# Kernel tuning notes

Hardware: AMD Instinct MI355X
Metric: run time of the kernel (lower is better)

Reference implementation:

```python
import jax, jax.numpy as jnp
import numpy as np

N = 100000
E = 1600000
IN_DIM = 128
HID = 128
OUT = 64
BN_EPS = 1e-5


def setup_inputs() -> dict:
    key = jax.random.key(0)
    ks = jax.random.split(key, 12)
    x = jax.random.normal(ks[0], (N, IN_DIM), dtype=jnp.float32)
    src = jax.random.randint(ks[1], (E,), 0, N, dtype=jnp.int64)
    dst = jax.random.randint(ks[2], (E,), 0, N, dtype=jnp.int64)
    edge_index = jnp.stack([src, dst], axis=0)
    def glorot(k, fan_in, fan_out):
        s = jnp.sqrt(6.0 / (fan_in + fan_out)).astype(jnp.float32)
        return jax.random.uniform(k, (fan_in, fan_out), jnp.float32, -s, s)
    return {
        "x": x,
        "edge_index": edge_index,
        "W1": glorot(ks[3], IN_DIM, HID), "b1": jnp.zeros((HID,), jnp.float32),
        "g1": jnp.ones((HID,), jnp.float32), "be1": jnp.zeros((HID,), jnp.float32),
        "W2": glorot(ks[4], HID, HID), "b2": jnp.zeros((HID,), jnp.float32),
        "g2": jnp.ones((HID,), jnp.float32), "be2": jnp.zeros((HID,), jnp.float32),
        "W3": glorot(ks[5], HID, OUT), "b3": jnp.zeros((OUT,), jnp.float32),
    }


def _gcn_norm(edge_index, n):
    # PyG GCNConv: add self-loops, symmetric normalization D^-1/2 (A+I) D^-1/2
    loop = jnp.arange(n, dtype=edge_index.dtype)
    src = jnp.concatenate([edge_index[0], loop])
    dst = jnp.concatenate([edge_index[1], loop])
    deg = jax.ops.segment_sum(jnp.ones_like(src, dtype=jnp.float32), dst, num_segments=n)
    dinv = jnp.where(deg > 0, jax.lax.rsqrt(deg), 0.0)
    norm = dinv[src] * dinv[dst]  # [E+N]
    return src, dst, norm


def _gcn(x, src, dst, norm, W, b, n):
    xw = x @ W                                  # [N, out]
    msg = xw[src] * norm[:, None]               # gather over edges
    return jax.ops.segment_sum(msg, dst, num_segments=n) + b


def _bn(x, g, be):
    # training-mode BatchNorm1d over node dim, biased variance
    mu = jnp.mean(x, axis=0)
    var = jnp.mean(jnp.square(x - mu), axis=0)
    return (x - mu) * jax.lax.rsqrt(var + BN_EPS) * g + be


def reference(x, edge_index, W1, b1, g1, be1, W2, b2, g2, be2, W3, b3):
    n = x.shape[0]
    src, dst, norm = _gcn_norm(edge_index, n)
    h = _gcn(x, src, dst, norm, W1, b1, n)
    h = jax.nn.relu(_bn(h, g1, be1))  # dropout = identity (eval)
    h = _gcn(h, src, dst, norm, W2, b2, n)
    h = jax.nn.relu(_bn(h, g2, be2))
    return _gcn(h, src, dst, norm, W3, b3, n)
```

## Files before the change

### kernel.cpp

```cpp
#include <hip/hip_runtime.h>
#include <cstdint>
#include <cstddef>

#define BN_EPS 1e-5f
#define BKT 256
#define BSH 9
#define CHUNK 8192

typedef __attribute__((ext_vector_type(8))) short bf16x8;
typedef __attribute__((ext_vector_type(4))) float f32x4;

__device__ __forceinline__ unsigned int f32_to_bf16_rne(float f) {
    unsigned int u = __float_as_uint(f);
    u += 0x7FFFu + ((u >> 16) & 1u);
    return u >> 16;
}
__device__ __forceinline__ unsigned int pack_bf16x2(float a, float b) {
    return f32_to_bf16_rne(a) | (f32_to_bf16_rne(b) << 16);
}
__device__ __forceinline__ float bf16_lo(unsigned int p) { return __uint_as_float(p << 16); }
__device__ __forceinline__ float bf16_hi(unsigned int p) { return __uint_as_float(p & 0xFFFF0000u); }

__global__ void hist_kernel(const int* __restrict__ dst, int* __restrict__ H, int e, int G) {
    __shared__ int h[BKT];
    int t = threadIdx.x, g = blockIdx.x;
    h[t] = 0;
    __syncthreads();
    int base = g * CHUNK;
#pragma unroll
    for (int i = 0; i < CHUNK / 256; i++) {
        int idx = base + i * 256 + t;
        if (idx < e) atomicAdd(&h[dst[idx] >> BSH], 1);
    }
    __syncthreads();
    H[t * G + g] = h[t];
}

__global__ void bin_scatter_kernel(const int* __restrict__ src, const int* __restrict__ dst,
                                   const int* __restrict__ Hscan, uint2* __restrict__ binned,
                                   int e, int G) {
    __shared__ int cur[BKT];
    int t = threadIdx.x, g = blockIdx.x;
    cur[t] = Hscan[t * G + g];
    __syncthreads();
    int base = g * CHUNK;
#pragma unroll
    for (int i = 0; i < CHUNK / 256; i++) {
        int idx = base + i * 256 + t;
        if (idx < e) {
            int s = src[idx], d = dst[idx];
            int pos = atomicAdd(&cur[d >> BSH], 1);
            uint2 v; v.x = (unsigned)s; v.y = (unsigned)d;
            binned[pos] = v;
        }
    }
}

__global__ __launch_bounds__(256) void bucket_build_kernel(const uint2* __restrict__ binned,
                                                           const int* __restrict__ Hscan,
                                                           int* __restrict__ cnt,
                                                           int* __restrict__ rowptr,
                                                           float* __restrict__ dinv,
                                                           int* __restrict__ esrc,
                                                           int e, int G, int n) {
    __shared__ int lcnt[512], lexc[512], ssum[256];
    const int t = threadIdx.x;
    const int b = blockIdx.x;
    const int start = Hscan[b * G];
    const int end = (b == BKT - 1) ? e : Hscan[(b + 1) * G];

    lcnt[t] = 0; lcnt[t + 256] = 0;
    __syncthreads();
    for (int i = start + t; i < end; i += 256)
        atomicAdd(&lcnt[binned[i].y & 511], 1);
    __syncthreads();

    int a0 = lcnt[2 * t], a1 = lcnt[2 * t + 1];
    ssum[t] = a0 + a1;
    __syncthreads();
    for (int off = 1; off < 256; off <<= 1) {
        int v = (t >= off) ? ssum[t - off] : 0;
        __syncthreads();
        ssum[t] += v;
        __syncthreads();
    }
    int excl = (t == 0) ? 0 : ssum[t - 1];
    lexc[2 * t] = excl;
    lexc[2 * t + 1] = excl + a0;
    __syncthreads();

    int nodebase = b << BSH;
#pragma unroll
    for (int j2 = 0; j2 < 2; j2++) {
        int j = 2 * t + j2;
        int node = nodebase + j;
        if (node < n) {
            int c = lcnt[j];
            cnt[node] = c;
            rowptr[node] = start + lexc[j];
            dinv[node] = rsqrtf((float)(c + 1));
        }
    }
    __syncthreads();

    for (int i = start + t; i < end; i += 256) {
        uint2 ed = binned[i];
        int pos = start + atomicAdd(&lexc[ed.y & 511], 1);
        esrc[pos] = (int)ed.x;
    }
}


__global__ void blocksum_kernel(const int* __restrict__ in, int* __restrict__ bsum, int n) {
    int t = threadIdx.x;
    int base = blockIdx.x * 1024 + t * 4;
    int s = 0;
    if (base + 3 < n) {
        int4 v = *(const int4*)&in[base];
        s = v.x + v.y + v.z + v.w;
    } else {
        for (int j = 0; j < 4; j++) if (base + j < n) s += in[base + j];
    }
    __shared__ int ls[256];
    ls[t] = s;
    __syncthreads();
    for (int off = 128; off > 0; off >>= 1) {
        if (t < off) ls[t] += ls[t + off];
        __syncthreads();
    }
    if (t == 0) bsum[blockIdx.x] = ls[0];
}

__global__ void scan_bsum_kernel(int* __restrict__ bsum, int nb) {
    int t = threadIdx.x;
    __shared__ int ls[256];
    int v = (t < nb) ? bsum[t] : 0;
    ls[t] = v;
    __syncthreads();
    for (int off = 1; off < 256; off <<= 1) {
        int p = (t >= off) ? ls[t - off] : 0;
        __syncthreads();
        ls[t] += p;
        __syncthreads();
    }
    if (t < nb) bsum[t] = ls[t] - v;
}

__global__ void scan_write1_kernel(const int* __restrict__ in, const int* __restrict__ bsum,
                                   int* __restrict__ out, int n) {
    int t = threadIdx.x;
    int base = blockIdx.x * 1024 + t * 4;
    int v[4];
    int s = 0;
    if (base + 3 < n) {
        int4 q = *(const int4*)&in[base];
        v[0] = q.x; v[1] = q.y; v[2] = q.z; v[3] = q.w;
        s = q.x + q.y + q.z + q.w;
    } else {
        for (int j = 0; j < 4; j++) { v[j] = (base + j < n) ? in[base + j] : 0; s += v[j]; }
    }
    __shared__ int ls[256];
    ls[t] = s;
    __syncthreads();
    for (int off = 1; off < 256; off <<= 1) {
        int p = (t >= off) ? ls[t - off] : 0;
        __syncthreads();
        ls[t] += p;
        __syncthreads();
    }
    int run = bsum[blockIdx.x] + ls[t] - s;
    if (base + 3 < n) {
        int4 r; r.x = run; r.y = run + v[0]; r.z = run + v[0] + v[1]; r.w = run + v[0] + v[1] + v[2];
        *(int4*)&out[base] = r;
    } else {
        for (int j = 0; j < 4; j++) {
            if (base + j < n) out[base + j] = run;
            run += v[j];
        }
    }
}


__device__ __forceinline__ void wprep_one(const float* __restrict__ W,
                                          uint4* __restrict__ whi, uint4* __restrict__ wlo,
                                          int slot, int OUTC) {
    int l  = slot & 63;
    int kc = (slot >> 6) & 3;
    int ct = slot >> 8;
    int c  = ct * 16 + (l & 15);
    int k0 = kc * 32 + (l >> 4) * 8;
    unsigned hi[4], lo[4];
#pragma unroll
    for (int jj = 0; jj < 4; jj++) {
        float v0 = W[(size_t)(k0 + 2 * jj) * OUTC + c];
        float v1 = W[(size_t)(k0 + 2 * jj + 1) * OUTC + c];
        unsigned h0 = f32_to_bf16_rne(v0), h1 = f32_to_bf16_rne(v1);
        float l0 = v0 - __uint_as_float(h0 << 16);
        float l1 = v1 - __uint_as_float(h1 << 16);
        hi[jj] = h0 | (h1 << 16);
        lo[jj] = pack_bf16x2(l0, l1);
    }
    uint4 uh; uh.x = hi[0]; uh.y = hi[1]; uh.z = hi[2]; uh.w = hi[3];
    uint4 ul; ul.x = lo[0]; ul.y = lo[1]; ul.z = lo[2]; ul.w = lo[3];
    whi[slot] = uh;
    wlo[slot] = ul;
}

__global__ void wprep_all_kernel(const float* __restrict__ W1, uint4* w1hi, uint4* w1lo,
                                 const float* __restrict__ W2, uint4* w2hi, uint4* w2lo,
                                 const float* __restrict__ W3, uint4* w3hi, uint4* w3lo) {
    int id = blockIdx.x * 256 + threadIdx.x;
    if (id < 2048)       wprep_one(W1, w1hi, w1lo, id, 128);
    else if (id < 4096)  wprep_one(W2, w2hi, w2lo, id - 2048, 128);
    else if (id < 5120)  wprep_one(W3, w3hi, w3lo, id - 4096, 64);
}


template <int OUTC>
__global__ __launch_bounds__(256) void gemm_kernel(const float* __restrict__ X,
                                                   const uint4* __restrict__ whi,
                                                   const uint4* __restrict__ wlo,
                                                   const float* __restrict__ scale,
                                                   const float* __restrict__ shift,
                                                   const float* __restrict__ dinv,
                                                   unsigned int* __restrict__ Y, int n) {
    constexpr int NCT = OUTC / 16;
    constexpr int CTW = NCT / 4;
    __shared__ __align__(16) unsigned short lAhi[64 * 128];
    __shared__ __align__(16) unsigned short lAlo[64 * 128];
    __shared__ float ldv[64];
    const int t = threadIdx.x;
    const int base = blockIdx.x * 64;
    const int lane = t & 63;
    const int w = t >> 6;
    const bool bn = (scale != nullptr);

    if (t < 64) { int r = base + t; ldv[t] = (r < n) ? dinv[r] : 0.0f; }

    bf16x8 bhi[CTW][4], blo[CTW][4];
#pragma unroll
    for (int c = 0; c < CTW; c++) {
        int ct = w * CTW + c;
#pragma unroll
        for (int kc = 0; kc < 4; kc++) {
            int slot = (ct * 4 + kc) * 64 + lane;
            bhi[c][kc] = *reinterpret_cast<const bf16x8*>(whi + slot);
            blo[c][kc] = *reinterpret_cast<const bf16x8*>(wlo + slot);
        }
    }

    const int col4 = (t & 31) * 4;
    float4 sc4, sh4;
    if (bn) {
        sc4 = *(const float4*)&scale[col4];
        sh4 = *(const float4*)&shift[col4];
    }
#pragma unroll
    for (int i = 0; i < 8; i++) {
        int row = i * 8 + (t >> 5);
        int r = base + row;
        float4 xv = make_float4(0.f, 0.f, 0.f, 0.f);
        if (r < n) xv = *(const float4*)&X[(size_t)r * 128 + col4];
        if (bn) {
            xv.x = fmaxf(fmaf(xv.x, sc4.x, sh4.x), 0.0f);
            xv.y = fmaxf(fmaf(xv.y, sc4.y, sh4.y), 0.0f);
            xv.z = fmaxf(fmaf(xv.z, sc4.z, sh4.z), 0.0f);
            xv.w = fmaxf(fmaf(xv.w, sc4.w, sh4.w), 0.0f);
        }
        unsigned h0 = f32_to_bf16_rne(xv.x), h1 = f32_to_bf16_rne(xv.y);
        unsigned h2 = f32_to_bf16_rne(xv.z), h3 = f32_to_bf16_rne(xv.w);
        float l0 = xv.x - __uint_as_float(h0 << 16);
        float l1 = xv.y - __uint_as_float(h1 << 16);
        float l2 = xv.z - __uint_as_float(h2 << 16);
        float l3 = xv.w - __uint_as_float(h3 << 16);
        uint2 ph; ph.x = h0 | (h1 << 16); ph.y = h2 | (h3 << 16);
        uint2 pl; pl.x = pack_bf16x2(l0, l1); pl.y = pack_bf16x2(l2, l3);
        int off = row * 256 + ((col4 * 2) ^ ((row & 7) << 4));
        *(uint2*)((char*)lAhi + off) = ph;
        *(uint2*)((char*)lAlo + off) = pl;
    }
    __syncthreads();

    const int arow = lane & 15;
    const int kb16 = (lane >> 4) * 16;
#pragma unroll
    for (int rt = 0; rt < 4; rt++) {
        f32x4 acc[CTW];
#pragma unroll
        for (int c = 0; c < CTW; c++) acc[c] = (f32x4){0.f, 0.f, 0.f, 0.f};
        int row = rt * 16 + arow;
        int rb = row * 256;
        int sw = (row & 7) << 4;
#pragma unroll
        for (int kc = 0; kc < 4; kc++) {
            int off = rb + ((kc * 64 + kb16) ^ sw);
            bf16x8 ah = *(const bf16x8*)((const char*)lAhi + off);
            bf16x8 al = *(const bf16x8*)((const char*)lAlo + off);
#pragma unroll
            for (int c = 0; c < CTW; c++) {
                acc[c] = __builtin_amdgcn_mfma_f32_16x16x32_bf16(bhi[c][kc], ah, acc[c], 0, 0, 0);
                acc[c] = __builtin_amdgcn_mfma_f32_16x16x32_bf16(blo[c][kc], ah, acc[c], 0, 0, 0);
                acc[c] = __builtin_amdgcn_mfma_f32_16x16x32_bf16(bhi[c][kc], al, acc[c], 0, 0, 0);
            }
        }
        int r = base + row;
        if (r < n) {
            float dv = ldv[row];
#pragma unroll
            for (int c = 0; c < CTW; c++) {
                int ct = w * CTW + c;
                uint2 o;
                o.x = pack_bf16x2(acc[c][0] * dv, acc[c][1] * dv);
                o.y = pack_bf16x2(acc[c][2] * dv, acc[c][3] * dv);
                *(uint2*)&Y[(size_t)r * (OUTC / 2) + ct * 8 + (lane >> 4) * 2] = o;
            }
        }
    }
}


__global__ __launch_bounds__(256) void agg128_kernel(const unsigned int* __restrict__ xw,
                                                     const int* __restrict__ rowptr,
                                                     const int* __restrict__ cnt,
                                                     const int* __restrict__ esrc,
                                                     const float* __restrict__ dinv,
                                                     const float* __restrict__ bias,
                                                     float* __restrict__ out,
                                                     float* __restrict__ bnpart, int n) {
    __shared__ float lp[8][128];
    __shared__ float lq[8][128];

    const uint2* xw2 = (const uint2*)xw;
    int wid = (blockIdx.x * 256 + threadIdx.x) >> 6;
    int lane = threadIdx.x & 63;
    int half = lane >> 5;
    int hl = lane & 31;
    int node = wid * 2 + half;
    bool ok = node < n;
    int nc = ok ? node : 0;

    float di = dinv[nc];
    int beg = rowptr[nc];
    int cv  = ok ? cnt[nc] : 0;
    int last = beg + cv - 1;
    int nb = (cv + 7) >> 3;

    uint2 ap = xw2[(size_t)nc * 32 + hl];
    float ax = bf16_lo(ap.x), ay = bf16_hi(ap.x);
    float az = bf16_lo(ap.y), aw = bf16_hi(ap.y);

    int s[8], sn[8];
    if (nb > 0) {
#pragma unroll
        for (int j = 0; j < 8; j++) {
            int idx = beg + j;
            s[j] = esrc[idx <= last ? idx : last];
        }
    }
    for (int b = 0; b < nb; b++) {
        int ebase = beg + b * 8;
        if (b + 1 < nb) {
#pragma unroll
            for (int j = 0; j < 8; j++) {
                int idx = ebase + 8 + j;
                sn[j] = esrc[idx <= last ? idx : last];
            }
        }
        uint2 v[8];
#pragma unroll
        for (int j = 0; j < 8; j++) v[j] = xw2[(size_t)s[j] * 32 + hl];
        int rem = last - ebase;
#pragma unroll
        for (int j = 0; j < 8; j++) {
            float m = (j <= rem) ? 1.0f : 0.0f;
            ax = fmaf(m, bf16_lo(v[j].x), ax);
            ay = fmaf(m, bf16_hi(v[j].x), ay);
            az = fmaf(m, bf16_lo(v[j].y), az);
            aw = fmaf(m, bf16_hi(v[j].y), aw);
        }
        if (b + 1 < nb) {
#pragma unroll
            for (int j = 0; j < 8; j++) s[j] = sn[j];
        }
    }

    float4 o = make_float4(0.f, 0.f, 0.f, 0.f);
    if (ok) {
        float4 bv = ((const float4*)bias)[hl];
        o.x = fmaf(di, ax, bv.x);
        o.y = fmaf(di, ay, bv.y);
        o.z = fmaf(di, az, bv.z);
        o.w = fmaf(di, aw, bv.w);
        ((float4*)(out + (size_t)node * 128))[hl] = o;
    }

    int row8 = (threadIdx.x >> 6) * 2 + half;
    int c0 = hl * 4;
    lp[row8][c0 + 0] = o.x;  lq[row8][c0 + 0] = o.x * o.x;
    lp[row8][c0 + 1] = o.y;  lq[row8][c0 + 1] = o.y * o.y;
    lp[row8][c0 + 2] = o.z;  lq[row8][c0 + 2] = o.z * o.z;
    lp[row8][c0 + 3] = o.w;  lq[row8][c0 + 3] = o.w * o.w;
    __syncthreads();
    int c = threadIdx.x & 127;
    int which = threadIdx.x >> 7;
    float srd = 0.0f;
#pragma unroll
    for (int r = 0; r < 8; r++) srd += which ? lq[r][c] : lp[r][c];
    bnpart[(size_t)blockIdx.x * 256 + threadIdx.x] = srd;
}


__global__ __launch_bounds__(256) void agg64_kernel(const unsigned int* __restrict__ xw,
                                                    const int* __restrict__ rowptr,
                                                    const int* __restrict__ cnt,
                                                    const int* __restrict__ esrc,
                                                    const float* __restrict__ dinv,
                                                    const float* __restrict__ bias,
                                                    float* __restrict__ out, int n) {
    int wid = (blockIdx.x * 256 + threadIdx.x) >> 6;
    int lane = threadIdx.x & 63;
    int half = lane >> 5;
    int hl = lane & 31;
    int node = wid * 2 + half;
    bool ok = node < n;
    int nc = ok ? node : 0;

    float di = dinv[nc];
    int beg = rowptr[nc];
    int cv  = ok ? cnt[nc] : 0;
    int last = beg + cv - 1;
    int nb = (cv + 7) >> 3;

    unsigned int ap = xw[(size_t)nc * 32 + hl];
    float ax = bf16_lo(ap), ay = bf16_hi(ap);

    int s[8], sn[8];
    if (nb > 0) {
#pragma unroll
        for (int j = 0; j < 8; j++) {
            int idx = beg + j;
            s[j] = esrc[idx <= last ? idx : last];
        }
    }
    for (int b = 0; b < nb; b++) {
        int ebase = beg + b * 8;
        if (b + 1 < nb) {
#pragma unroll
            for (int j = 0; j < 8; j++) {
                int idx = ebase + 8 + j;
                sn[j] = esrc[idx <= last ? idx : last];
            }
        }
        unsigned int v[8];
#pragma unroll
        for (int j = 0; j < 8; j++) v[j] = xw[(size_t)s[j] * 32 + hl];
        int rem = last - ebase;
#pragma unroll
        for (int j = 0; j < 8; j++) {
            float m = (j <= rem) ? 1.0f : 0.0f;
            ax = fmaf(m, bf16_lo(v[j]), ax);
            ay = fmaf(m, bf16_hi(v[j]), ay);
        }
        if (b + 1 < nb) {
#pragma unroll
            for (int j = 0; j < 8; j++) s[j] = sn[j];
        }
    }
    if (ok) {
        float2 bv = ((const float2*)bias)[hl];
        float2 o;
        o.x = fmaf(di, ax, bv.x);
        o.y = fmaf(di, ay, bv.y);
        ((float2*)(out + (size_t)node * 64))[hl] = o;
    }
}


__global__ void bnred_partial_kernel(const float* __restrict__ part, float* __restrict__ sums,
                                     int nblk) {
    int t = threadIdx.x;
    float s = 0.0f;
    for (int r = blockIdx.x; r < nblk; r += gridDim.x)
        s += part[(size_t)r * 256 + t];
    atomicAdd(&sums[t], s);
}

__global__ void bn_finalize_kernel(const float* __restrict__ sums, const float* __restrict__ g,
                                   const float* __restrict__ be, float* __restrict__ scale,
                                   float* __restrict__ shift, int n) {
    int c = threadIdx.x;
    float inv_n = 1.0f / (float)n;
    float mean = sums[c] * inv_n;
    float var = sums[128 + c] * inv_n - mean * mean;
    float rstd = rsqrtf(var + BN_EPS);
    float sc = rstd * g[c];
    scale[c] = sc;
    shift[c] = be[c] - mean * sc;
}


extern "C" void kernel_launch(void* const* d_in, const int* in_sizes, int n_in,
                              void* d_out, int out_size, void* d_ws, size_t ws_size,
                              hipStream_t stream) {
    const float* x   = (const float*)d_in[0];
    const int*   ei  = (const int*)d_in[1];
    const float* W1  = (const float*)d_in[2];
    const float* b1  = (const float*)d_in[3];
    const float* g1  = (const float*)d_in[4];
    const float* be1 = (const float*)d_in[5];
    const float* W2  = (const float*)d_in[6];
    const float* b2  = (const float*)d_in[7];
    const float* g2  = (const float*)d_in[8];
    const float* be2 = (const float*)d_in[9];
    const float* W3  = (const float*)d_in[10];
    const float* b3  = (const float*)d_in[11];

    const int n = in_sizes[0] / 128;
    const int E = in_sizes[1] / 2;
    const int* srcv = ei;
    const int* dstv = ei + E;

    const int G = (E + CHUNK - 1) / CHUNK;
    const int HN = BKT * G;
    const int NB = (n + 511) >> 9;

    char* p = (char*)d_ws;
    auto carve = [&](size_t bytes) -> char* {
        char* q = p;
        p += (bytes + 255) & ~(size_t)255;
        return q;
    };
    int*   cnt    = (int*)carve((size_t)n * 4);
    int*   rowptr = (int*)carve((size_t)n * 4);
    float* dinv   = (float*)carve((size_t)n * 4);
    int*   esrc   = (int*)carve((size_t)E * 4);
    uint2* binned = (uint2*)carve((size_t)E * 8);
    int*   H      = (int*)carve((size_t)HN * 4);
    int*   Hscan  = (int*)carve((size_t)HN * 4);
    float* sums   = (float*)carve(512 * 4);
    float* bnsc   = (float*)carve(512 * 4);
    int*   bsum   = (int*)carve(1024 * 4);
    uint4* w1hi   = (uint4*)carve(2048 * 16);
    uint4* w1lo   = (uint4*)carve(2048 * 16);
    uint4* w2hi   = (uint4*)carve(2048 * 16);
    uint4* w2lo   = (uint4*)carve(2048 * 16);
    uint4* w3hi   = (uint4*)carve(1024 * 16);
    uint4* w3lo   = (uint4*)carve(1024 * 16);
    unsigned int* xwb = (unsigned int*)carve((size_t)n * 128 * 2);
    float* bufB   = (float*)carve((size_t)n * 128 * 4);

    float* bnpart = (float*)binned;

    hipMemsetAsync(sums, 0, 512 * 4, stream);

    int sbH = (HN + 1023) / 1024;

    wprep_all_kernel<<<20, 256, 0, stream>>>(W1, w1hi, w1lo, W2, w2hi, w2lo, W3, w3hi, w3lo);

    hist_kernel<<<G, 256, 0, stream>>>(dstv, H, E, G);
    blocksum_kernel<<<sbH, 256, 0, stream>>>(H, bsum, HN);
    scan_bsum_kernel<<<1, 256, 0, stream>>>(bsum, sbH);
    scan_write1_kernel<<<sbH, 256, 0, stream>>>(H, bsum, Hscan, HN);
    bin_scatter_kernel<<<G, 256, 0, stream>>>(srcv, dstv, Hscan, binned, E, G);
    bucket_build_kernel<<<NB, 256, 0, stream>>>(binned, Hscan, cnt, rowptr, dinv, esrc, E, G, n);

    int gb = (n + 63) / 64;
    int ab = (n + 7) / 8;

    gemm_kernel<128><<<gb, 256, 0, stream>>>(x, w1hi, w1lo, nullptr, nullptr, dinv, xwb, n);
    agg128_kernel<<<ab, 256, 0, stream>>>(xwb, rowptr, cnt, esrc, dinv, b1, bufB, bnpart, n);
    bnred_partial_kernel<<<64, 256, 0, stream>>>(bnpart, sums, ab);
    bn_finalize_kernel<<<1, 128, 0, stream>>>(sums, g1, be1, bnsc, bnsc + 128, n);

    gemm_kernel<128><<<gb, 256, 0, stream>>>(bufB, w2hi, w2lo, bnsc, bnsc + 128, dinv, xwb, n);
    agg128_kernel<<<ab, 256, 0, stream>>>(xwb, rowptr, cnt, esrc, dinv, b2, bufB, bnpart, n);
    bnred_partial_kernel<<<64, 256, 0, stream>>>(bnpart, sums + 256, ab);
    bn_finalize_kernel<<<1, 128, 0, stream>>>(sums + 256, g2, be2, bnsc + 256, bnsc + 384, n);

    gemm_kernel<64><<<gb, 256, 0, stream>>>(bufB, w3hi, w3lo, bnsc + 256, bnsc + 384, dinv, xwb, n);
    agg64_kernel<<<ab, 256, 0, stream>>>(xwb, rowptr, cnt, esrc, dinv, b3, (float*)d_out, n);
}
```

Baseline: 502.8 us.

## Store 128-wide GEMM output in column slabs and aggregate per slab

```diff
diff --git a/kernel.cpp b/kernel.cpp
--- a/kernel.cpp
+++ b/kernel.cpp
@@ -216,7 +216,7 @@
 }
 
 
-template <int OUTC>
+template <int OUTC, bool SLAB>
 __global__ __launch_bounds__(256) void gemm_kernel(const float* __restrict__ X,
                                                    const uint4* __restrict__ whi,
                                                    const uint4* __restrict__ wlo,
@@ -312,30 +312,37 @@
                 uint2 o;
                 o.x = pack_bf16x2(acc[c][0] * dv, acc[c][1] * dv);
                 o.y = pack_bf16x2(acc[c][2] * dv, acc[c][3] * dv);
-                *(uint2*)&Y[(size_t)r * (OUTC / 2) + ct * 8 + (lane >> 4) * 2] = o;
+                if constexpr (SLAB)
+                    *(uint2*)&Y[(size_t)ct * n * 8 + (size_t)r * 8 + (lane >> 4) * 2] = o;
+                else
+                    *(uint2*)&Y[(size_t)r * (OUTC / 2) + ct * 8 + (lane >> 4) * 2] = o;
             }
         }
     }
 }
 
 
-__global__ __launch_bounds__(256) void agg128_kernel(const unsigned int* __restrict__ xw,
-                                                     const int* __restrict__ rowptr,
-                                                     const int* __restrict__ cnt,
-                                                     const int* __restrict__ esrc,
-                                                     const float* __restrict__ dinv,
-                                                     const float* __restrict__ bias,
-                                                     float* __restrict__ out,
-                                                     float* __restrict__ bnpart, int n) {
-    __shared__ float lp[8][128];
-    __shared__ float lq[8][128];
+__global__ __launch_bounds__(256) void agg128s_kernel(const unsigned int* __restrict__ xw,
+                                                      const int* __restrict__ rowptr,
+                                                      const int* __restrict__ cnt,
+                                                      const int* __restrict__ esrc,
+                                                      const float* __restrict__ dinv,
+                                                      const float* __restrict__ bias,
+                                                      float* __restrict__ out,
+                                                      float* __restrict__ bnpart, int n) {
+    __shared__ float lp[64][16], lq[64][16];
+    __shared__ float lr[2][16][8];
 
     const uint2* xw2 = (const uint2*)xw;
-    int wid = (blockIdx.x * 256 + threadIdx.x) >> 6;
-    int lane = threadIdx.x & 63;
-    int half = lane >> 5;
-    int hl = lane & 31;
-    int node = wid * 2 + half;
+    const int slab = blockIdx.x & 7;
+    const int grp  = blockIdx.x >> 3;
+    const int t = threadIdx.x;
+    const int w = t >> 6;
+    const int lane = t & 63;
+    const int slot = lane >> 2;
+    const int sub  = lane & 3;
+    const int lnode = w * 16 + slot;
+    const int node = grp * 64 + lnode;
     bool ok = node < n;
     int nc = ok ? node : 0;
 
@@ -345,7 +352,8 @@
     int last = beg + cv - 1;
     int nb = (cv + 7) >> 3;
 
-    uint2 ap = xw2[(size_t)nc * 32 + hl];
+    const size_t sbase = (size_t)slab * n * 4;
+    uint2 ap = xw2[sbase + (size_t)nc * 4 + sub];
     float ax = bf16_lo(ap.x), ay = bf16_hi(ap.x);
     float az = bf16_lo(ap.y), aw = bf16_hi(ap.y);
 
@@ -368,7 +376,7 @@
         }
         uint2 v[8];
 #pragma unroll
-        for (int j = 0; j < 8; j++) v[j] = xw2[(size_t)s[j] * 32 + hl];
+        for (int j = 0; j < 8; j++) v[j] = xw2[sbase + (size_t)s[j] * 4 + sub];
         int rem = last - ebase;
 #pragma unroll
         for (int j = 0; j < 8; j++) {
@@ -386,27 +394,41 @@
 
     float4 o = make_float4(0.f, 0.f, 0.f, 0.f);
     if (ok) {
-        float4 bv = ((const float4*)bias)[hl];
+        float4 bv = ((const float4*)bias)[slab * 4 + sub];
         o.x = fmaf(di, ax, bv.x);
         o.y = fmaf(di, ay, bv.y);
         o.z = fmaf(di, az, bv.z);
         o.w = fmaf(di, aw, bv.w);
-        ((float4*)(out + (size_t)node * 128))[hl] = o;
-    }
-
-    int row8 = (threadIdx.x >> 6) * 2 + half;
-    int c0 = hl * 4;
-    lp[row8][c0 + 0] = o.x;  lq[row8][c0 + 0] = o.x * o.x;
-    lp[row8][c0 + 1] = o.y;  lq[row8][c0 + 1] = o.y * o.y;
-    lp[row8][c0 + 2] = o.z;  lq[row8][c0 + 2] = o.z * o.z;
-    lp[row8][c0 + 3] = o.w;  lq[row8][c0 + 3] = o.w * o.w;
-    __syncthreads();
-    int c = threadIdx.x & 127;
-    int which = threadIdx.x >> 7;
-    float srd = 0.0f;
-#pragma unroll
-    for (int r = 0; r < 8; r++) srd += which ? lq[r][c] : lp[r][c];
-    bnpart[(size_t)blockIdx.x * 256 + threadIdx.x] = srd;
+        *(float4*)(out + (size_t)node * 128 + slab * 16 + sub * 4) = o;
+    }
+
+    int c0 = sub * 4;
+    lp[lnode][c0 + 0] = o.x;  lq[lnode][c0 + 0] = o.x * o.x;
+    lp[lnode][c0 + 1] = o.y;  lq[lnode][c0 + 1] = o.y * o.y;
+    lp[lnode][c0 + 2] = o.z;  lq[lnode][c0 + 2] = o.z * o.z;
+    lp[lnode][c0 + 3] = o.w;  lq[lnode][c0 + 3] = o.w * o.w;
+    __syncthreads();
+    {
+        int col = t & 15;
+        int which = (t >> 4) & 1;
+        int chunk = t >> 5;
+        float srd = 0.0f;
+#pragma unroll
+        for (int r = 0; r < 8; r++) {
+            int rr = chunk * 8 + r;
+            srd += which ? lq[rr][col] : lp[rr][col];
+        }
+        lr[which][col][chunk] = srd;
+    }
+    __syncthreads();
+    if (t < 32) {
+        int which = t >> 4;
+        int col = t & 15;
+        float srd = 0.0f;
+#pragma unroll
+        for (int c = 0; c < 8; c++) srd += lr[which][col][c];
+        bnpart[(size_t)blockIdx.x * 32 + which * 16 + col] = srd;
+    }
 }
 
 
@@ -476,13 +498,16 @@
 }
 
 
-__global__ void bnred_partial_kernel(const float* __restrict__ part, float* __restrict__ sums,
-                                     int nblk) {
+__global__ void bnred_slab_kernel(const float* __restrict__ part, float* __restrict__ sums,
+                                  int ngrp) {
     int t = threadIdx.x;
+    int which = t >> 7;
+    int c = t & 127;
+    int slab = c >> 4, lcol = c & 15;
     float s = 0.0f;
-    for (int r = blockIdx.x; r < nblk; r += gridDim.x)
-        s += part[(size_t)r * 256 + t];
-    atomicAdd(&sums[t], s);
+    for (int k = blockIdx.x; k < ngrp; k += gridDim.x)
+        s += part[(size_t)(k * 8 + slab) * 32 + which * 16 + lcol];
+    atomicAdd(&sums[which * 128 + c], s);
 }
 
 __global__ void bn_finalize_kernel(const float* __restrict__ sums, const float* __restrict__ g,
@@ -565,18 +590,19 @@
     bucket_build_kernel<<<NB, 256, 0, stream>>>(binned, Hscan, cnt, rowptr, dinv, esrc, E, G, n);
 
     int gb = (n + 63) / 64;
+    int ngrp = (n + 63) / 64;
     int ab = (n + 7) / 8;
 
-    gemm_kernel<128><<<gb, 256, 0, stream>>>(x, w1hi, w1lo, nullptr, nullptr, dinv, xwb, n);
-    agg128_kernel<<<ab, 256, 0, stream>>>(xwb, rowptr, cnt, esrc, dinv, b1, bufB, bnpart, n);
-    bnred_partial_kernel<<<64, 256, 0, stream>>>(bnpart, sums, ab);
+    gemm_kernel<128, true><<<gb, 256, 0, stream>>>(x, w1hi, w1lo, nullptr, nullptr, dinv, xwb, n);
+    agg128s_kernel<<<ngrp * 8, 256, 0, stream>>>(xwb, rowptr, cnt, esrc, dinv, b1, bufB, bnpart, n);
+    bnred_slab_kernel<<<64, 256, 0, stream>>>(bnpart, sums, ngrp);
     bn_finalize_kernel<<<1, 128, 0, stream>>>(sums, g1, be1, bnsc, bnsc + 128, n);
 
-    gemm_kernel<128><<<gb, 256, 0, stream>>>(bufB, w2hi, w2lo, bnsc, bnsc + 128, dinv, xwb, n);
-    agg128_kernel<<<ab, 256, 0, stream>>>(xwb, rowptr, cnt, esrc, dinv, b2, bufB, bnpart, n);
-    bnred_partial_kernel<<<64, 256, 0, stream>>>(bnpart, sums + 256, ab);
+    gemm_kernel<128, true><<<gb, 256, 0, stream>>>(bufB, w2hi, w2lo, bnsc, bnsc + 128, dinv, xwb, n);
+    agg128s_kernel<<<ngrp * 8, 256, 0, stream>>>(xwb, rowptr, cnt, esrc, dinv, b2, bufB, bnpart, n);
+    bnred_slab_kernel<<<64, 256, 0, stream>>>(bnpart, sums + 256, ngrp);
     bn_finalize_kernel<<<1, 128, 0, stream>>>(sums + 256, g2, be2, bnsc + 256, bnsc + 384, n);
 
-    gemm_kernel<64><<<gb, 256, 0, stream>>>(bufB, w3hi, w3lo, bnsc + 256, bnsc + 384, dinv, xwb, n);
+    gemm_kernel<64, false><<<gb, 256, 0, stream>>>(bufB, w3hi, w3lo, bnsc + 256, bnsc + 384, dinv, xwb, n);
     agg64_kernel<<<ab, 256, 0, stream>>>(xwb, rowptr, cnt, esrc, dinv, b3, (float*)d_out, n);
 }
```

Result: faster. 445.7 us (-11.4%).
